# Optimization experiments

Hardware: AMD Instinct MI355X
Metric: run time of the kernel (lower is better)

Reference implementation:

```python
import jax, jax.numpy as jnp
import numpy as np

EMBED = 1024
HEADS = 16
HEAD_DIM = EMBED // HEADS
LN_EPS = 1e-5


def setup_inputs() -> dict:
    key = jax.random.key(0)
    ks = jax.random.split(key, 7)
    B, S = 2, 2048
    x = jax.random.normal(ks[0], (B, S, EMBED), dtype=jnp.float32)
    attn_params = jax.random.uniform(ks[1], (B, S, 3 * EMBED), dtype=jnp.float32)
    sc = 1.0 / np.sqrt(EMBED)
    Wqkv = jax.random.normal(ks[2], (3 * EMBED, EMBED), dtype=jnp.float32) * sc
    Wout = jax.random.normal(ks[3], (EMBED, EMBED), dtype=jnp.float32) * sc
    b_out = jnp.zeros((EMBED,), dtype=jnp.float32)
    gamma = jnp.ones((EMBED,), dtype=jnp.float32)
    beta = jnp.zeros((EMBED,), dtype=jnp.float32)
    return {"x": x, "attn_params": attn_params, "Wqkv": Wqkv, "Wout": Wout,
            "b_out": b_out, "gamma": gamma, "beta": beta}


def reference(x, attn_params, Wqkv, Wout, b_out, gamma, beta):
    B, S, E = x.shape
    # qkv projection (no bias) followed by elementwise attn_params scaling
    qkv = jnp.einsum('bse,fe->bsf', x, Wqkv) * attn_params  # [B,S,3E]
    q, k, v = jnp.split(qkv, 3, axis=-1)
    # [B,H,S,D]
    q = q.reshape(B, S, HEADS, HEAD_DIM).transpose(0, 2, 1, 3)
    k = k.reshape(B, S, HEADS, HEAD_DIM).transpose(0, 2, 1, 3)
    v = v.reshape(B, S, HEADS, HEAD_DIM).transpose(0, 2, 1, 3)
    scores = jnp.einsum('bhqd,bhkd->bhqk', q, k) / jnp.sqrt(jnp.float32(HEAD_DIM))
    attn = jax.nn.softmax(scores, axis=-1)
    weighted = jnp.einsum('bhqk,bhkd->bhqd', attn, v)  # [B,H,S,D]
    weighted = weighted.transpose(0, 2, 1, 3).reshape(B, S, E)
    out = jnp.einsum('bse,fe->bsf', weighted, Wout) + b_out
    out = out + x  # residual
    # layernorm over last dim
    mu = jnp.mean(out, axis=-1, keepdims=True)
    var = jnp.mean(jnp.square(out - mu), axis=-1, keepdims=True)
    return (out - mu) * jax.lax.rsqrt(var + LN_EPS) * gamma + beta
```

## Files before the change

kernel.cpp:

```cpp
#include <hip/hip_runtime.h>

typedef float f32x4 __attribute__((ext_vector_type(4)));
typedef short s16x8 __attribute__((ext_vector_type(8)));
typedef unsigned short u16;

#define AS1 __attribute__((address_space(1)))
#define AS3 __attribute__((address_space(3)))

__device__ __forceinline__ u16 f2bf(float f){
    union { float f; unsigned u; } v; v.f = f;
    unsigned r = v.u + 0x7FFFu + ((v.u >> 16) & 1u);
    return (u16)(r >> 16);
}

__device__ __forceinline__ void pswap(unsigned &A, unsigned &B){
    asm("v_permlane32_swap_b32 %0, %1\n\tv_permlane16_swap_b32 %0, %1" : "+v"(A), "+v"(B));
}
__device__ __forceinline__ unsigned cvtpk(float lo, float hi){
    unsigned w;
    asm("v_cvt_pk_bf16_f32 %0, %1, %2" : "=v"(w) : "v"(lo), "v"(hi));
    return w;
}

__global__ __launch_bounds__(256) void cvt3_bf16(
    const float* __restrict__ a, u16* __restrict__ da, int na,
    const float* __restrict__ b, u16* __restrict__ db, int nb,
    const float* __restrict__ c, u16* __restrict__ dc, int nc)
{
    int i = blockIdx.x * 256 + threadIdx.x;
    const float* s; u16* d; int off;
    if (i < na){ s = a; d = da; off = i; }
    else if (i < na + nb){ s = b; d = db; off = i - na; }
    else if (i < na + nb + nc){ s = c; d = dc; off = i - na - nb; }
    else return;
    float4 v = ((const float4*)s)[off];
    ushort4 o;
    o.x = f2bf(v.x); o.y = f2bf(v.y); o.z = f2bf(v.z); o.w = f2bf(v.w);
    ((ushort4*)d)[off] = o;
}

__global__ __launch_bounds__(512, 2) void gemm256(
    const u16* __restrict__ A, const u16* __restrict__ Bw,
    int N, int K,
    const float* __restrict__ e0, u16* __restrict__ Cout)
{
    __shared__ u16 lds[2][4][128 * 64];
    const int tid = threadIdx.x;
    const int w = tid >> 6, l = tid & 63;
    const int g = l >> 4, c = l & 15;
    const int wm = w >> 2, wn = w & 3;
    const int nbh = 2 + (wn >> 1);
    const int nb = wn & 1;
    const int sg = (g ^ (((c >> 3) & 1) << 1) ^ ((c >> 2) & 1)) << 4;

    const int bid = blockIdx.x;
    const int xcd = bid & 7, lin = bid >> 3;
    const int rowBase = (xcd * 2 + (lin & 1)) * 256;
    const int colBase = (lin >> 1) * 256;

    const int s_r_lo = l >> 2;
    const int s_col  = ((l & 3) ^ (((l >> 5) & 1) << 1) ^ ((l >> 4) & 1)) * 8;

    f32x4 acc[8][4] = {};

#define STAGE_HALF(bb, hh, j_) do{                                                         \
    const u16* Gb_ = ((hh) < 2) ? (A + (size_t)(rowBase + (hh) * 128) * K)                 \
                                : (Bw + (size_t)(colBase + ((hh) - 2) * 128) * K);         \
    _Pragma("unroll")                                                                      \
    for (int i_ = 0; i_ < 2; ++i_){                                                        \
        int st_ = i_ * 8 + w;                                                              \
        int r_  = (st_ >> 1) * 16 + s_r_lo;                                                \
        int col_ = (st_ & 1) * 32 + s_col;                                                 \
        const u16* src_ = Gb_ + (size_t)r_ * K + ((j_) * 64 + col_);                       \
        __builtin_amdgcn_global_load_lds((const AS1 void*)src_,                            \
            (AS3 void*)((char*)&lds[bb][hh][0] + (i_ * 8 + w) * 1024), 16, 0, 0);          \
    } }while(0)

#define LDA4(bb, mh) do{                                                                   \
    _Pragma("unroll") for (int mi_ = 0; mi_ < 4; ++mi_){                                   \
        _Pragma("unroll") for (int kk_ = 0; kk_ < 2; ++kk_){                               \
            int mt_ = (mh) * 4 + mi_;                                                      \
            a2[mi_][kk_] = *(const s16x8*)((const char*)&lds[bb][wm][0] +                  \
                (((mt_ * 2 + kk_) << 10) + c * 64 + sg));                                  \
        } } }while(0)

#define LDB2(bb, nh) do{                                                                   \
    _Pragma("unroll") for (int ni_ = 0; ni_ < 2; ++ni_){                                   \
        _Pragma("unroll") for (int kk_ = 0; kk_ < 2; ++kk_){                               \
            int nt_ = (nh) * 2 + ni_;                                                      \
            bfr[nh][ni_][kk_] = *(const s16x8*)((const char*)&lds[bb][nbh][0] +            \
                ((((nb * 4 + nt_) * 2 + kk_) << 10) + c * 64 + sg));                       \
        } } }while(0)

#define MFMA16(mh, nh) do{                                                                 \
    __builtin_amdgcn_s_setprio(1);                                                         \
    _Pragma("unroll") for (int mi_ = 0; mi_ < 4; ++mi_){                                   \
        _Pragma("unroll") for (int ni_ = 0; ni_ < 2; ++ni_){                               \
            _Pragma("unroll") for (int kk_ = 0; kk_ < 2; ++kk_){                           \
                acc[(mh)*4+mi_][(nh)*2+ni_] = __builtin_amdgcn_mfma_f32_16x16x32_bf16(     \
                    a2[mi_][kk_], bfr[nh][ni_][kk_], acc[(mh)*4+mi_][(nh)*2+ni_], 0,0,0);  \
            } } }                                                                          \
    __builtin_amdgcn_s_setprio(0);                                                         \
}while(0)

    const int ntk = K >> 6;
    STAGE_HALF(0, 0, 0); STAGE_HALF(0, 1, 0); STAGE_HALF(0, 2, 0); STAGE_HALF(0, 3, 0);
    __syncthreads();

    s16x8 a2[4][2];
    s16x8 bfr[2][2][2];
    for (int j = 0; j < ntk; ++j){
        const int cur = j & 1, nxt = cur ^ 1;
        const bool pf = (j + 1 < ntk);
        LDA4(cur, 0);
        LDB2(cur, 0);
        if (pf){ STAGE_HALF(nxt, 0, j + 1); STAGE_HALF(nxt, 1, j + 1); }
        MFMA16(0, 0);
        LDB2(cur, 1);
        if (pf) STAGE_HALF(nxt, 2, j + 1);
        MFMA16(0, 1);
        LDA4(cur, 1);
        if (pf) STAGE_HALF(nxt, 3, j + 1);
        MFMA16(1, 1);
        MFMA16(1, 0);
        __syncthreads();
    }

#pragma unroll
    for (int mt = 0; mt < 8; ++mt){
        const int rbase = rowBase + wm * 128 + mt * 16 + g * 4;
        float ev[16];
#pragma unroll
        for (int nt_ = 0; nt_ < 4; ++nt_){
            const int cc = colBase + wn * 64 + nt_ * 16 + c;
#pragma unroll
            for (int jj = 0; jj < 4; ++jj)
                ev[nt_ * 4 + jj] = e0[(size_t)(rbase + jj) * N + cc];
        }
#pragma unroll
        for (int nt_ = 0; nt_ < 4; ++nt_){
            const int cc = colBase + wn * 64 + nt_ * 16 + c;
#pragma unroll
            for (int jj = 0; jj < 4; ++jj){
                float apv = ev[nt_ * 4 + jj];
                if (cc < 1024) apv *= 0.18033688f;
                Cout[(size_t)(rbase + jj) * N + cc] = f2bf(acc[mt][nt_][jj] * apv);
            }
        }
    }
#undef STAGE_HALF
#undef LDA4
#undef LDB2
#undef MFMA16
}

__global__ __launch_bounds__(256) void gemm_bt(
    const u16* __restrict__ A, const u16* __restrict__ Bw,
    int M, int N, int K,
    const float* __restrict__ e0, const float* __restrict__ e1,
    float* __restrict__ Cout)
{
    __shared__ u16 As[2][128 * 32];
    __shared__ u16 Bs[2][128 * 32];
    const int tid = threadIdx.x;
    const int w = tid >> 6, lane = tid & 63;
    const int g = lane >> 4, c = lane & 15;
    const int wr = w >> 1, wc = w & 1;
    const int rowBase = blockIdx.y * 128;
    const int colBase = blockIdx.x * 128;

    f32x4 acc[4][4] = {};

    auto STAGE = [&](int pb, int k0){
#pragma unroll
        for (int i = 0; i < 2; ++i){
            int o  = i * 4096 + tid * 16;
            int r  = o >> 6;
            int ce = (o & 63) >> 1;
            const u16* ga = A  + (size_t)(rowBase + r) * K + (k0 + ce);
            __builtin_amdgcn_global_load_lds((const AS1 void*)ga,
                (AS3 void*)((char*)As[pb] + i * 4096 + w * 1024), 16, 0, 0);
            const u16* gb = Bw + (size_t)(colBase + r) * K + (k0 + ce);
            __builtin_amdgcn_global_load_lds((const AS1 void*)gb,
                (AS3 void*)((char*)Bs[pb] + i * 4096 + w * 1024), 16, 0, 0);
        }
    };

    const int nt = K >> 5;
    STAGE(0, 0);
    __syncthreads();

    for (int t = 0; t < nt; ++t){
        const int cur = t & 1;
        if (t + 1 < nt) STAGE(cur ^ 1, (t + 1) * 32);

        s16x8 af[4], bfr[4];
#pragma unroll
        for (int m = 0; m < 4; ++m){
            int row = wr * 64 + m * 16 + c;
            af[m] = *(const s16x8*)((const char*)As[cur] + row * 64 + g * 16);
        }
#pragma unroll
        for (int n = 0; n < 4; ++n){
            int row = wc * 64 + n * 16 + c;
            bfr[n] = *(const s16x8*)((const char*)Bs[cur] + row * 64 + g * 16);
        }
#pragma unroll
        for (int m = 0; m < 4; ++m)
#pragma unroll
            for (int n = 0; n < 4; ++n)
                acc[m][n] = __builtin_amdgcn_mfma_f32_16x16x32_bf16(af[m], bfr[n], acc[m][n], 0, 0, 0);
        __syncthreads();
    }

    float bcol[4];
#pragma unroll
    for (int n = 0; n < 4; ++n)
        bcol[n] = e0[colBase + wc * 64 + n * 16 + c];

#pragma unroll
    for (int m = 0; m < 4; ++m){
        const int rbase = rowBase + wr * 64 + m * 16 + g * 4;
        float ev[16];
#pragma unroll
        for (int n = 0; n < 4; ++n){
            const int cc = colBase + wc * 64 + n * 16 + c;
#pragma unroll
            for (int j = 0; j < 4; ++j)
                ev[n * 4 + j] = e1[(size_t)(rbase + j) * N + cc];
        }
#pragma unroll
        for (int n = 0; n < 4; ++n){
            const int cc = colBase + wc * 64 + n * 16 + c;
#pragma unroll
            for (int j = 0; j < 4; ++j)
                Cout[(size_t)(rbase + j) * N + cc] = acc[m][n][j] + bcol[n] + ev[n * 4 + j];
        }
    }
}

__global__ __launch_bounds__(256) void vtrans(const u16* __restrict__ qkv, u16* __restrict__ vt){
    __shared__ u16 t_[64 * 64];
    int bh = blockIdx.x; int b = bh >> 4; int h = bh & 15;
    int st = blockIdx.y;
    int tid = threadIdx.x;
#pragma unroll
    for (int i = 0; i < 2; ++i){
        int id = i * 256 + tid;
        int sr = id >> 3, c8 = id & 7;
        uint4 v = *(const uint4*)(qkv + (size_t)(b * 2048 + st * 64 + sr) * 3072 + 2048 + h * 64 + c8 * 8);
        *(uint4*)((char*)t_ + ((sr * 128 + c8 * 16) ^ ((sr & 7) << 4))) = v;
    }
    __syncthreads();
#pragma unroll
    for (int i = 0; i < 2; ++i){
        int id = i * 256 + tid;
        int d = id >> 3, s8 = (id & 7) * 8;
        u16 tmp[8];
#pragma unroll
        for (int jj = 0; jj < 8; ++jj){
            int s = s8 + jj;
            tmp[jj] = *(const u16*)((const char*)t_ + ((s * 128 + d * 2) ^ ((s & 7) << 4)));
        }
        *(uint4*)(vt + ((size_t)bh * 64 + d) * 2048 + st * 64 + s8) = *(uint4*)tmp;
    }
}

__global__ __launch_bounds__(512) void attn_k(const u16* __restrict__ qkv,
                                              const u16* __restrict__ vt,
                                              u16* __restrict__ o)
{
    __shared__ u16 Kl[2][64 * 64];
    __shared__ u16 Vl[2][64 * 64];
    int bh = blockIdx.x; int b = bh >> 4, h = bh & 15;
    int qt = blockIdx.y;
    int tid = threadIdx.x;
    int w = tid >> 6, lane = tid & 63, g = lane >> 4, c = lane & 15;

    const size_t qrow = (size_t)(b * 2048 + qt * 128 + w * 16 + c);
    s16x8 qf[2];
    qf[0] = *(const s16x8*)(qkv + qrow * 3072 + h * 64 + g * 8);
    qf[1] = *(const s16x8*)(qkv + qrow * 3072 + h * 64 + 32 + g * 8);

    const s16x8 ones8 = {16256, 16256, 16256, 16256, 16256, 16256, 16256, 16256};

    f32x4 oa[4] = {};
    f32x4 la = {};

    int kr = tid >> 3, c8 = tid & 7;
    const u16* kg = qkv + (size_t)(b * 2048 + kr) * 3072 + 1024 + h * 64 + c8 * 8;
    const u16* vg = vt + ((size_t)bh * 64 + kr) * 2048 + c8 * 8;
    const int so = (kr * 128 + c8 * 16) ^ ((kr & 7) << 4);

    uint4 ks = *(const uint4*)kg;
    uint4 vs = *(const uint4*)vg;
    *(uint4*)((char*)Kl[0] + so) = ks;
    *(uint4*)((char*)Vl[0] + so) = vs;
    __syncthreads();

    for (int t = 0; t < 32; ++t){
        const int cur = t & 1;
        if (t < 31){
            ks = *(const uint4*)(kg + (size_t)(t + 1) * 64 * 3072);
            vs = *(const uint4*)(vg + (t + 1) * 64);
        }

        f32x4 st[4];
        __builtin_amdgcn_s_setprio(1);
#pragma unroll
        for (int kt = 0; kt < 4; ++kt){
            int row = kt * 16 + c;
            s16x8 kf0 = *(const s16x8*)((const char*)Kl[cur] + ((row * 128 + g * 16) ^ ((row & 7) << 4)));
            s16x8 kf1 = *(const s16x8*)((const char*)Kl[cur] + ((row * 128 + 64 + g * 16) ^ ((row & 7) << 4)));
            f32x4 a = {};
            a = __builtin_amdgcn_mfma_f32_16x16x32_bf16(kf0, qf[0], a, 0, 0, 0);
            a = __builtin_amdgcn_mfma_f32_16x16x32_bf16(kf1, qf[1], a, 0, 0, 0);
            st[kt] = a;
        }
        __builtin_amdgcn_s_setprio(0);

        unsigned W[4][2];
#pragma unroll
        for (int kt = 0; kt < 4; ++kt){
            float p0 = __builtin_amdgcn_exp2f(st[kt][0]);
            float p1 = __builtin_amdgcn_exp2f(st[kt][1]);
            float p2 = __builtin_amdgcn_exp2f(st[kt][2]);
            float p3 = __builtin_amdgcn_exp2f(st[kt][3]);
            W[kt][0] = cvtpk(p0, p1);
            W[kt][1] = cvtpk(p2, p3);
        }

        __builtin_amdgcn_s_setprio(1);
#pragma unroll
        for (int kb = 0; kb < 2; ++kb){
            unsigned t0 = W[kb * 2][0], t2 = W[kb * 2 + 1][0];
            pswap(t0, t2);
            unsigned t1 = W[kb * 2][1], t3 = W[kb * 2 + 1][1];
            pswap(t1, t3);
            union { unsigned u[4]; s16x8 v; } pu;
            pu.u[0] = t0; pu.u[1] = t1; pu.u[2] = t2; pu.u[3] = t3;
#pragma unroll
            for (int dt = 0; dt < 4; ++dt){
                int vrow = dt * 16 + c;
                s16x8 vf = *(const s16x8*)((const char*)Vl[cur] + ((vrow * 128 + kb * 64 + g * 16) ^ ((vrow & 7) << 4)));
                oa[dt] = __builtin_amdgcn_mfma_f32_16x16x32_bf16(vf, pu.v, oa[dt], 0, 0, 0);
            }
            la = __builtin_amdgcn_mfma_f32_16x16x32_bf16(ones8, pu.v, la, 0, 0, 0);
        }
        __builtin_amdgcn_s_setprio(0);

        if (t < 31){
            *(uint4*)((char*)Kl[cur ^ 1] + so) = ks;
            *(uint4*)((char*)Vl[cur ^ 1] + so) = vs;
        }
        __syncthreads();
    }

    float inv = 1.0f / la[0];
#pragma unroll
    for (int dt = 0; dt < 4; ++dt){
        u16 t4[4];
#pragma unroll
        for (int j = 0; j < 4; ++j) t4[j] = f2bf(oa[dt][j] * inv);
        *(uint2*)(o + qrow * 1024 + h * 64 + dt * 16 + g * 4) = *(uint2*)t4;
    }
}

__global__ __launch_bounds__(256) void ln_k(const float* __restrict__ tmp,
                                            const float* __restrict__ gamma,
                                            const float* __restrict__ beta,
                                            float* __restrict__ out)
{
    int row = blockIdx.x;
    int tid = threadIdx.x;
    float4 v = ((const float4*)(tmp + (size_t)row * 1024))[tid];
    float s  = v.x + v.y + v.z + v.w;
    float ss = v.x * v.x + v.y * v.y + v.z * v.z + v.w * v.w;
    for (int m = 1; m < 64; m <<= 1){ s += __shfl_xor(s, m); ss += __shfl_xor(ss, m); }
    __shared__ float red[8];
    int w = tid >> 6;
    if ((tid & 63) == 0){ red[w * 2] = s; red[w * 2 + 1] = ss; }
    __syncthreads();
    s  = red[0] + red[2] + red[4] + red[6];
    ss = red[1] + red[3] + red[5] + red[7];
    float mu  = s * (1.f / 1024.f);
    float var = ss * (1.f / 1024.f) - mu * mu;
    float inv = rsqrtf(var + 1e-5f);
    float4 g4 = ((const float4*)gamma)[tid];
    float4 b4 = ((const float4*)beta)[tid];
    float4 r;
    r.x = (v.x - mu) * inv * g4.x + b4.x;
    r.y = (v.y - mu) * inv * g4.y + b4.y;
    r.z = (v.z - mu) * inv * g4.z + b4.z;
    r.w = (v.w - mu) * inv * g4.w + b4.w;
    ((float4*)(out + (size_t)row * 1024))[tid] = r;
}

extern "C" void kernel_launch(void* const* d_in, const int* in_sizes, int n_in,
                              void* d_out, int out_size, void* d_ws, size_t ws_size,
                              hipStream_t stream)
{
    const float* x     = (const float*)d_in[0];
    const float* ap    = (const float*)d_in[1];
    const float* wqkv  = (const float*)d_in[2];
    const float* wout  = (const float*)d_in[3];
    const float* bout  = (const float*)d_in[4];
    const float* gamma = (const float*)d_in[5];
    const float* beta  = (const float*)d_in[6];
    float* out = (float*)d_out;

    char* ws = (char*)d_ws;
    u16* xb    = (u16*)ws;  ws += (size_t)4096 * 1024 * 2;
    u16* wqkvb = (u16*)ws;  ws += (size_t)3072 * 1024 * 2;
    u16* woutb = (u16*)ws;  ws += (size_t)1024 * 1024 * 2;
    u16* qkvb  = (u16*)ws;  ws += (size_t)4096 * 3072 * 2;
    u16* vtb   = (u16*)ws;  ws += (size_t)32 * 64 * 2048 * 2;
    u16* attnb = (u16*)ws;  ws += (size_t)4096 * 1024 * 2;
    float* tmp = (float*)ws;

    const int na = 4096 * 1024 / 4, nb = 3072 * 1024 / 4, nc = 1024 * 1024 / 4;
    cvt3_bf16<<<(na + nb + nc + 255) / 256, 256, 0, stream>>>(x, xb, na, wqkv, wqkvb, nb, wout, woutb, nc);

    gemm256<<<192, 512, 0, stream>>>(xb, wqkvb, 3072, 1024, ap, qkvb);
    vtrans<<<dim3(32, 32), 256, 0, stream>>>(qkvb, vtb);
    attn_k<<<dim3(32, 16), 512, 0, stream>>>(qkvb, vtb, attnb);
    gemm_bt<<<dim3(8, 32), 256, 0, stream>>>(attnb, woutb, 4096, 1024, 1024, bout, x, tmp);
    ln_k<<<4096, 256, 0, stream>>>(tmp, gamma, beta, out);
}
```

Before: 127.9 us.

## Fuse V transpose into QKV GEMM epilogue and load B fragments from global

The QKV GEMM epilogue now writes the V third of the output directly in transposed [bh,d,s] layout, so the separate vtrans kernel and its extra read and write pass are removed. The GEMM also stops staging the weight tile through LDS. Each wave loads its B fragments straight from global memory into double-buffered registers, which halves LDS use and the staging traffic. In exchange, B reads are no longer shared across the waves of a block, register pressure rises, and the transposed V stores are narrow 8-byte writes.

```diff
diff --git a/kernel.cpp b/kernel.cpp
--- a/kernel.cpp
+++ b/kernel.cpp
@@ -42,15 +42,13 @@
 __global__ __launch_bounds__(512, 2) void gemm256(
     const u16* __restrict__ A, const u16* __restrict__ Bw,
     int N, int K,
-    const float* __restrict__ e0, u16* __restrict__ Cout)
-{
-    __shared__ u16 lds[2][4][128 * 64];
+    const float* __restrict__ e0, u16* __restrict__ Cout, u16* __restrict__ Vt)
+{
+    __shared__ u16 lds[2][2][128 * 64];
     const int tid = threadIdx.x;
     const int w = tid >> 6, l = tid & 63;
     const int g = l >> 4, c = l & 15;
     const int wm = w >> 2, wn = w & 3;
-    const int nbh = 2 + (wn >> 1);
-    const int nb = wn & 1;
     const int sg = (g ^ (((c >> 3) & 1) << 1) ^ ((c >> 2) & 1)) << 4;
 
     const int bid = blockIdx.x;
@@ -63,9 +61,10 @@
 
     f32x4 acc[8][4] = {};
 
-#define STAGE_HALF(bb, hh, j_) do{                                                         \
-    const u16* Gb_ = ((hh) < 2) ? (A + (size_t)(rowBase + (hh) * 128) * K)                 \
-                                : (Bw + (size_t)(colBase + ((hh) - 2) * 128) * K);         \
+    const u16* Bbase = Bw + (size_t)(colBase + wn * 64 + c) * K + g * 8;
+
+#define STAGE_A(bb, hh, j_) do{                                                            \
+    const u16* Gb_ = A + (size_t)(rowBase + (hh) * 128) * K;                               \
     _Pragma("unroll")                                                                      \
     for (int i_ = 0; i_ < 2; ++i_){                                                        \
         int st_ = i_ * 8 + w;                                                              \
@@ -73,7 +72,7 @@
         int col_ = (st_ & 1) * 32 + s_col;                                                 \
         const u16* src_ = Gb_ + (size_t)r_ * K + ((j_) * 64 + col_);                       \
         __builtin_amdgcn_global_load_lds((const AS1 void*)src_,                            \
-            (AS3 void*)((char*)&lds[bb][hh][0] + (i_ * 8 + w) * 1024), 16, 0, 0);          \
+            (AS3 void*)((char*)&lds[bb][hh][0] + st_ * 1024), 16, 0, 0);                   \
     } }while(0)
 
 #define LDA4(bb, mh) do{                                                                   \
@@ -84,48 +83,60 @@
                 (((mt_ * 2 + kk_) << 10) + c * 64 + sg));                                  \
         } } }while(0)
 
-#define LDB2(bb, nh) do{                                                                   \
-    _Pragma("unroll") for (int ni_ = 0; ni_ < 2; ++ni_){                                   \
+#define LDB_G(dst, j_) do{                                                                 \
+    _Pragma("unroll") for (int nt_ = 0; nt_ < 4; ++nt_){                                   \
         _Pragma("unroll") for (int kk_ = 0; kk_ < 2; ++kk_){                               \
-            int nt_ = (nh) * 2 + ni_;                                                      \
-            bfr[nh][ni_][kk_] = *(const s16x8*)((const char*)&lds[bb][nbh][0] +            \
-                ((((nb * 4 + nt_) * 2 + kk_) << 10) + c * 64 + sg));                       \
+            dst[nt_][kk_] = *(const s16x8*)(Bbase + (size_t)nt_ * 16 * K +                 \
+                ((j_) * 64 + kk_ * 32));                                                   \
         } } }while(0)
 
-#define MFMA16(mh, nh) do{                                                                 \
+#define MFMA16(mh, nh, Bf) do{                                                             \
     __builtin_amdgcn_s_setprio(1);                                                         \
     _Pragma("unroll") for (int mi_ = 0; mi_ < 4; ++mi_){                                   \
         _Pragma("unroll") for (int ni_ = 0; ni_ < 2; ++ni_){                               \
             _Pragma("unroll") for (int kk_ = 0; kk_ < 2; ++kk_){                           \
                 acc[(mh)*4+mi_][(nh)*2+ni_] = __builtin_amdgcn_mfma_f32_16x16x32_bf16(     \
-                    a2[mi_][kk_], bfr[nh][ni_][kk_], acc[(mh)*4+mi_][(nh)*2+ni_], 0,0,0);  \
+                    a2[mi_][kk_], Bf[(nh)*2+ni_][kk_], acc[(mh)*4+mi_][(nh)*2+ni_], 0,0,0);\
             } } }                                                                          \
     __builtin_amdgcn_s_setprio(0);                                                         \
 }while(0)
 
     const int ntk = K >> 6;
-    STAGE_HALF(0, 0, 0); STAGE_HALF(0, 1, 0); STAGE_HALF(0, 2, 0); STAGE_HALF(0, 3, 0);
+    s16x8 a2[4][2];
+    s16x8 bA[4][2], bB[4][2];
+
+    STAGE_A(0, 0, 0); STAGE_A(0, 1, 0);
+    LDB_G(bA, 0);
     __syncthreads();
 
-    s16x8 a2[4][2];
-    s16x8 bfr[2][2][2];
-    for (int j = 0; j < ntk; ++j){
-        const int cur = j & 1, nxt = cur ^ 1;
-        const bool pf = (j + 1 < ntk);
-        LDA4(cur, 0);
-        LDB2(cur, 0);
-        if (pf){ STAGE_HALF(nxt, 0, j + 1); STAGE_HALF(nxt, 1, j + 1); }
-        MFMA16(0, 0);
-        LDB2(cur, 1);
-        if (pf) STAGE_HALF(nxt, 2, j + 1);
-        MFMA16(0, 1);
-        LDA4(cur, 1);
-        if (pf) STAGE_HALF(nxt, 3, j + 1);
-        MFMA16(1, 1);
-        MFMA16(1, 0);
-        __syncthreads();
-    }
-
+    for (int j = 0; j < ntk; j += 2){
+        {
+            const bool pf = (j + 1 < ntk);
+            LDA4(0, 0);
+            if (pf){ LDB_G(bB, j + 1); STAGE_A(1, 0, j + 1); }
+            MFMA16(0, 0, bA);
+            MFMA16(0, 1, bA);
+            LDA4(0, 1);
+            if (pf) STAGE_A(1, 1, j + 1);
+            MFMA16(1, 1, bA);
+            MFMA16(1, 0, bA);
+            __syncthreads();
+        }
+        if (j + 1 < ntk){
+            const bool pf = (j + 2 < ntk);
+            LDA4(1, 0);
+            if (pf){ LDB_G(bA, j + 2); STAGE_A(0, 0, j + 2); }
+            MFMA16(0, 0, bB);
+            MFMA16(0, 1, bB);
+            LDA4(1, 1);
+            if (pf) STAGE_A(0, 1, j + 2);
+            MFMA16(1, 1, bB);
+            MFMA16(1, 0, bB);
+            __syncthreads();
+        }
+    }
+
+    const int bsel = (rowBase >= 2048) ? 1 : 0;
 #pragma unroll
     for (int mt = 0; mt < 8; ++mt){
         const int rbase = rowBase + wm * 128 + mt * 16 + g * 4;
@@ -140,17 +151,29 @@
 #pragma unroll
         for (int nt_ = 0; nt_ < 4; ++nt_){
             const int cc = colBase + wn * 64 + nt_ * 16 + c;
-#pragma unroll
-            for (int jj = 0; jj < 4; ++jj){
-                float apv = ev[nt_ * 4 + jj];
-                if (cc < 1024) apv *= 0.18033688f;
-                Cout[(size_t)(rbase + jj) * N + cc] = f2bf(acc[mt][nt_][jj] * apv);
+            if (cc < 2048){
+#pragma unroll
+                for (int jj = 0; jj < 4; ++jj){
+                    float apv = ev[nt_ * 4 + jj];
+                    if (cc < 1024) apv *= 0.18033688f;
+                    Cout[(size_t)(rbase + jj) * N + cc] = f2bf(acc[mt][nt_][jj] * apv);
+                }
+            } else {
+                u16 t4[4];
+#pragma unroll
+                for (int jj = 0; jj < 4; ++jj)
+                    t4[jj] = f2bf(acc[mt][nt_][jj] * ev[nt_ * 4 + jj]);
+                const int vcol = cc - 2048;
+                const int bh = bsel * 16 + (vcol >> 6);
+                const int d  = vcol & 63;
+                const int s  = rbase & 2047;
+                *(uint2*)(Vt + ((size_t)bh * 64 + d) * 2048 + s) = *(uint2*)t4;
             }
         }
     }
-#undef STAGE_HALF
+#undef STAGE_A
 #undef LDA4
-#undef LDB2
+#undef LDB_G
 #undef MFMA16
 }
 
@@ -236,33 +259,6 @@
             for (int j = 0; j < 4; ++j)
                 Cout[(size_t)(rbase + j) * N + cc] = acc[m][n][j] + bcol[n] + ev[n * 4 + j];
         }
-    }
-}
-
-__global__ __launch_bounds__(256) void vtrans(const u16* __restrict__ qkv, u16* __restrict__ vt){
-    __shared__ u16 t_[64 * 64];
-    int bh = blockIdx.x; int b = bh >> 4; int h = bh & 15;
-    int st = blockIdx.y;
-    int tid = threadIdx.x;
-#pragma unroll
-    for (int i = 0; i < 2; ++i){
-        int id = i * 256 + tid;
-        int sr = id >> 3, c8 = id & 7;
-        uint4 v = *(const uint4*)(qkv + (size_t)(b * 2048 + st * 64 + sr) * 3072 + 2048 + h * 64 + c8 * 8);
-        *(uint4*)((char*)t_ + ((sr * 128 + c8 * 16) ^ ((sr & 7) << 4))) = v;
-    }
-    __syncthreads();
-#pragma unroll
-    for (int i = 0; i < 2; ++i){
-        int id = i * 256 + tid;
-        int d = id >> 3, s8 = (id & 7) * 8;
-        u16 tmp[8];
-#pragma unroll
-        for (int jj = 0; jj < 8; ++jj){
-            int s = s8 + jj;
-            tmp[jj] = *(const u16*)((const char*)t_ + ((s * 128 + d * 2) ^ ((s & 7) << 4)));
-        }
-        *(uint4*)(vt + ((size_t)bh * 64 + d) * 2048 + st * 64 + s8) = *(uint4*)tmp;
     }
 }
 
@@ -421,8 +417,7 @@
     const int na = 4096 * 1024 / 4, nb = 3072 * 1024 / 4, nc = 1024 * 1024 / 4;
     cvt3_bf16<<<(na + nb + nc + 255) / 256, 256, 0, stream>>>(x, xb, na, wqkv, wqkvb, nb, wout, woutb, nc);
 
-    gemm256<<<192, 512, 0, stream>>>(xb, wqkvb, 3072, 1024, ap, qkvb);
-    vtrans<<<dim3(32, 32), 256, 0, stream>>>(qkvb, vtb);
+    gemm256<<<192, 512, 0, stream>>>(xb, wqkvb, 3072, 1024, ap, qkvb, vtb);
     attn_k<<<dim3(32, 16), 512, 0, stream>>>(qkvb, vtb, attnb);
     gemm_bt<<<dim3(8, 32), 256, 0, stream>>>(attnb, woutb, 4096, 1024, 1024, bout, x, tmp);
     ln_k<<<4096, 256, 0, stream>>>(tmp, gamma, beta, out);
```

New measurement: 143.4 us. +12.1%, slower.
